# Kernel tuning notes

Measured on AMD Instinct MI355X. Metric: run time of the kernel, lower is better.

Reference implementation:

```python
import jax, jax.numpy as jnp
import numpy as np

B, H, S, D = 4, 8, 8192, 64


def setup_inputs() -> dict:
    key = jax.random.key(0)
    kq, kk, kv_, kqm, kkm = jax.random.split(key, 5)
    q = jax.random.normal(kq, (B, H, S, D), dtype=jnp.float32)
    k = jax.random.normal(kk, (B, H, S, D), dtype=jnp.float32)
    v = jax.random.normal(kv_, (B, H, S, D), dtype=jnp.float32)
    q_mask = jax.random.randint(kqm, (B, S), 0, 2).astype(jnp.bool_)
    kv_mask = jax.random.randint(kkm, (B, S), 0, 2).astype(jnp.bool_)
    return {"q": q, "k": k, "v": v, "q_mask": q_mask, "kv_mask": kv_mask}


def reference(q, k, v, q_mask, kv_mask):
    # Linear (kernelized) attention branch: feature map phi(x) = elu(x) + 1
    qe = jax.nn.elu(q) + 1.0
    ke = jax.nn.elu(k) + 1.0
    qm = q_mask.astype(q.dtype)[:, None, :, None]   # [B,1,S,1]
    km = kv_mask.astype(q.dtype)[:, None, :, None]
    qe = qe * qm
    ke = ke * km
    ve = v * km
    s = v.shape[2]
    # kv: [B,H,D,D] contraction over kv sequence
    kv = jnp.einsum('bhsd,bhsc->bhdc', ke, ve / s)
    # normalizer per query position: [B,H,L]
    div = 1.0 / (jnp.einsum('bhld,bhsd->bhl', qe, ke) + 1e-6)
    out = s * jnp.einsum('bhld,bhdc,bhl->bhlc', qe, kv, div)
    return out
```

## Files before the change

### kernel.cpp

```cpp
#include <hip/hip_runtime.h>


#define S_LEN 8192
#define NBH 32
#define KVSTRIDE 4160
#define NCHUNK 16
#define K3_XB 16

typedef __attribute__((ext_vector_type(4))) float f32x4;

__device__ __forceinline__ float elu1(float x) {
  return x > 0.0f ? (x + 1.0f) : __expf(x);
}

__global__ __launch_bounds__(256) void k1_partial(
    const float* __restrict__ kin, const float* __restrict__ vin,
    const int* __restrict__ kv_mask, float* __restrict__ partials, int seg_rows) {
  __shared__ float ke_lds[2][64 * 64];
  __shared__ float ve_lds[2][64 * 64];
  const int tid = threadIdx.x;
  const int seg = blockIdx.x, bh = blockIdx.y, b = bh >> 3;
  const int rbase = seg * seg_rows;
  const int dg = tid >> 4, cg = tid & 15;
  const float* kbase = kin + (size_t)bh * S_LEN * 64;
  const float* vbase = vin + (size_t)bh * S_LEN * 64;
  const int* mbase = kv_mask + b * S_LEN;

  f32x4 kr[4], vr[4];
  float mr[4];
  float acc[4][4];
#pragma unroll
  for (int i = 0; i < 4; ++i)
#pragma unroll
    for (int j = 0; j < 4; ++j) acc[i][j] = 0.f;
  f32x4 ksump = {0.f, 0.f, 0.f, 0.f};

#define LOAD_T(r0_)                                                    \
  {                                                                    \
    const float* kp_ = kbase + (size_t)(r0_) * 64;                     \
    const float* vp_ = vbase + (size_t)(r0_) * 64;                     \
    _Pragma("unroll")                                                  \
    for (int i_ = 0; i_ < 4; ++i_) {                                   \
      int f_ = tid + 256 * i_;                                         \
      kr[i_] = *(const f32x4*)(kp_ + (size_t)f_ * 4);                  \
      vr[i_] = *(const f32x4*)(vp_ + (size_t)f_ * 4);                  \
      mr[i_] = mbase[(r0_) + dg + 16 * i_] ? 1.0f : 0.0f;              \
    }                                                                  \
  }

#define STORE_T(buf_)                                                  \
  {                                                                    \
    _Pragma("unroll")                                                  \
    for (int i_ = 0; i_ < 4; ++i_) {                                   \
      int row_ = dg + 16 * i_;                                         \
      float m_ = mr[i_];                                               \
      float mv_ = m_ * (1.0f / 8192.0f);                               \
      f32x4 ke4_, ve4_;                                                \
      _Pragma("unroll")                                                \
      for (int j_ = 0; j_ < 4; ++j_) {                                 \
        ke4_[j_] = elu1(kr[i_][j_]) * m_;                              \
        ve4_[j_] = vr[i_][j_] * mv_;                                   \
      }                                                                \
      ksump += ke4_;                                                   \
      *(f32x4*)&ke_lds[buf_][row_ * 64 + cg * 4] = ke4_;               \
      *(f32x4*)&ve_lds[buf_][row_ * 64 + cg * 4] = ve4_;               \
    }                                                                  \
  }

#define COMPUTE_T(buf_)                                                \
  {                                                                    \
    _Pragma("unroll 4")                                                \
    for (int s_ = 0; s_ < 64; ++s_) {                                  \
      f32x4 kd_ = *(const f32x4*)&ke_lds[buf_][s_ * 64 + dg * 4];      \
      f32x4 vc_ = *(const f32x4*)&ve_lds[buf_][s_ * 64 + cg * 4];      \
      _Pragma("unroll")                                                \
      for (int i_ = 0; i_ < 4; ++i_)                                   \
        _Pragma("unroll")                                              \
        for (int j_ = 0; j_ < 4; ++j_)                                 \
          acc[i_][j_] = fmaf(kd_[i_], vc_[j_], acc[i_][j_]);           \
    }                                                                  \
  }

  const int ntiles = seg_rows >> 6;
  LOAD_T(rbase)
  STORE_T(0)
  for (int t = 0; t < ntiles; ++t) {
    __syncthreads();
    if (t + 1 < ntiles) LOAD_T(rbase + (t + 1) * 64)
    COMPUTE_T(t & 1)
    if (t + 1 < ntiles) STORE_T((t + 1) & 1)
  }

  float* p = partials + ((size_t)bh * gridDim.x + seg) * KVSTRIDE;
#pragma unroll
  for (int i = 0; i < 4; ++i) {
    f32x4 o;
#pragma unroll
    for (int j = 0; j < 4; ++j) o[j] = acc[i][j];
    *(f32x4*)&p[(dg * 4 + i) * 64 + cg * 4] = o;
  }
  __syncthreads();
  *(f32x4*)&ke_lds[0][tid * 4] = ksump;
  __syncthreads();
  if (tid < 64) {
    float s = 0.f;
#pragma unroll
    for (int g = 0; g < 16; ++g)
      s += ke_lds[0][(g * 16 + (tid >> 2)) * 4 + (tid & 3)];
    p[4096 + tid] = s;
  }
#undef LOAD_T
#undef STORE_T
#undef COMPUTE_T
}

__global__ __launch_bounds__(256) void k2_reduce(
    const float* __restrict__ partials, float* __restrict__ kvg, int nchunk) {
  const int idx = blockIdx.x * 256 + threadIdx.x;
  if (idx >= NBH * KVSTRIDE) return;
  const int bh = idx / KVSTRIDE;
  const int e = idx - bh * KVSTRIDE;
  const float* p = partials + (size_t)bh * nchunk * KVSTRIDE + e;
  float s0 = 0.f, s1 = 0.f, s2 = 0.f, s3 = 0.f;
  int c = 0;
  for (; c + 4 <= nchunk; c += 4) {
    s0 += p[(size_t)(c + 0) * KVSTRIDE];
    s1 += p[(size_t)(c + 1) * KVSTRIDE];
    s2 += p[(size_t)(c + 2) * KVSTRIDE];
    s3 += p[(size_t)(c + 3) * KVSTRIDE];
  }
  for (; c < nchunk; ++c) s0 += p[(size_t)c * KVSTRIDE];
  kvg[idx] = (s0 + s1) + (s2 + s3);
}

__global__ __launch_bounds__(256) void k3_out(
    const float* __restrict__ qin, const int* __restrict__ q_mask,
    const float* __restrict__ kvg, float* __restrict__ out) {
  __shared__ float kv_lds[64 * 64];
  __shared__ float qe_lds[2][64 * 68];
  __shared__ float ks_lds[64];
  const int tid = threadIdx.x;
  const int xb = blockIdx.x, bh = blockIdx.y, b = bh >> 3;
  const int lg = tid >> 4, cg = tid & 15;
  const float* kvb = kvg + (size_t)bh * KVSTRIDE;
  const float* qb = qin + (size_t)bh * S_LEN * 64;
  const int* mb = q_mask + b * S_LEN;

#pragma unroll
  for (int i = 0; i < 4; ++i) {
    int f = tid + 256 * i;
    *(f32x4*)&kv_lds[f * 4] = *(const f32x4*)(kvb + (size_t)f * 4);
  }
  if (tid < 64) ks_lds[tid] = kvb[4096 + tid];

  f32x4 qr[4];
  float mr[4];

#define LOADQ(r0_)                                                     \
  {                                                                    \
    const float* qp_ = qb + (size_t)(r0_) * 64;                        \
    _Pragma("unroll")                                                  \
    for (int i_ = 0; i_ < 4; ++i_) {                                   \
      int f_ = tid + 256 * i_;                                         \
      qr[i_] = *(const f32x4*)(qp_ + (size_t)f_ * 4);                  \
      mr[i_] = mb[(r0_) + lg + 16 * i_] ? 1.0f : 0.0f;                 \
    }                                                                  \
  }

#define STOREQ(buf_)                                                   \
  {                                                                    \
    _Pragma("unroll")                                                  \
    for (int i_ = 0; i_ < 4; ++i_) {                                   \
      int row_ = lg + 16 * i_;                                         \
      float m_ = mr[i_];                                               \
      f32x4 qe_;                                                       \
      _Pragma("unroll")                                                \
      for (int j_ = 0; j_ < 4; ++j_) qe_[j_] = elu1(qr[i_][j_]) * m_;  \
      *(f32x4*)&qe_lds[buf_][row_ * 68 + cg * 4] = qe_;                \
    }                                                                  \
  }

  const int c0 = xb * 8;
  LOADQ(c0 * 64)
  STOREQ(0)
  for (int t = 0; t < 8; ++t) {
    __syncthreads();
    if (t + 1 < 8) LOADQ((c0 + t + 1) * 64)
    float acc[4][4];
    float den[4];
#pragma unroll
    for (int il = 0; il < 4; ++il) {
      den[il] = 0.f;
#pragma unroll
      for (int j = 0; j < 4; ++j) acc[il][j] = 0.f;
    }
    const float* qbuf = qe_lds[t & 1];
#pragma unroll 8
    for (int d = 0; d < 64; d += 2) {
      float2 ksv = *(const float2*)&ks_lds[d];
      f32x4 kv0 = *(const f32x4*)&kv_lds[d * 64 + cg * 4];
      f32x4 kv1 = *(const f32x4*)&kv_lds[(d + 1) * 64 + cg * 4];
#pragma unroll
      for (int il = 0; il < 4; ++il) {
        float2 qv = *(const float2*)&qbuf[(lg * 4 + il) * 68 + d];
        den[il] = fmaf(qv.x, ksv.x, fmaf(qv.y, ksv.y, den[il]));
#pragma unroll
        for (int j = 0; j < 4; ++j)
          acc[il][j] = fmaf(qv.x, kv0[j], fmaf(qv.y, kv1[j], acc[il][j]));
      }
    }
    if (t + 1 < 8) STOREQ((t + 1) & 1)
    const int r0 = (c0 + t) * 64;
#pragma unroll
    for (int il = 0; il < 4; ++il) {
      float inv = 8192.0f / (den[il] + 1e-6f);
      int row = r0 + lg * 4 + il;
      f32x4 o;
#pragma unroll
      for (int j = 0; j < 4; ++j) o[j] = acc[il][j] * inv;
      *(f32x4*)(out + ((size_t)bh * S_LEN + row) * 64 + cg * 4) = o;
    }
  }
#undef LOADQ
#undef STOREQ
}

extern "C" void kernel_launch(void* const* d_in, const int* in_sizes, int n_in,
                              void* d_out, int out_size, void* d_ws, size_t ws_size,
                              hipStream_t stream) {
  const float* q = (const float*)d_in[0];
  const float* k = (const float*)d_in[1];
  const float* v = (const float*)d_in[2];
  const int* qm = (const int*)d_in[3];
  const int* km = (const int*)d_in[4];
  float* out = (float*)d_out;

  int nchunk = NCHUNK;
  while (nchunk > 1) {
    size_t need = (size_t)NBH * nchunk * KVSTRIDE * 4 + (size_t)NBH * KVSTRIDE * 4;
    if (need <= ws_size) break;
    nchunk >>= 1;
  }
  float* partials = (float*)d_ws;
  float* kvg = partials + (size_t)NBH * nchunk * KVSTRIDE;
  int seg_rows = S_LEN / nchunk;

  k1_partial<<<dim3(nchunk, NBH), 256, 0, stream>>>(k, v, km, partials, seg_rows);
  int n_elem = NBH * KVSTRIDE;
  k2_reduce<<<dim3((n_elem + 255) / 256), 256, 0, stream>>>(partials, kvg, nchunk);
  k3_out<<<dim3(K3_XB, NBH), 256, 0, stream>>>(q, qm, kvg, out);
}
```

Measured before the change: 267.4 us.

## Single-buffer LDS and double grid blocks to raise occupancy in k1/k3

Replaces the double-buffered LDS tiles in the partial-KV and output kernels with single buffers, which adds an extra barrier per tile. It doubles the number of sequence chunks and output blocks per head and sets launch bounds to 4 blocks per CU. The goal is more resident blocks and more parallelism to hide global load latency. In exchange it loses the LDS double-buffer overlap, adds synchronization, and doubles the partials that the reduce kernel must sum.

```diff
diff --git a/kernel.cpp b/kernel.cpp
--- a/kernel.cpp
+++ b/kernel.cpp
@@ -4,8 +4,8 @@
 #define S_LEN 8192
 #define NBH 32
 #define KVSTRIDE 4160
-#define NCHUNK 16
-#define K3_XB 16
+#define NCHUNK 32
+#define K3_XB 32
 
 typedef __attribute__((ext_vector_type(4))) float f32x4;
 
@@ -13,11 +13,11 @@
   return x > 0.0f ? (x + 1.0f) : __expf(x);
 }
 
-__global__ __launch_bounds__(256) void k1_partial(
+__global__ __launch_bounds__(256, 4) void k1_partial(
     const float* __restrict__ kin, const float* __restrict__ vin,
     const int* __restrict__ kv_mask, float* __restrict__ partials, int seg_rows) {
-  __shared__ float ke_lds[2][64 * 64];
-  __shared__ float ve_lds[2][64 * 64];
+  __shared__ float ke_lds[64 * 64];
+  __shared__ float ve_lds[64 * 64];
   const int tid = threadIdx.x;
   const int seg = blockIdx.x, bh = blockIdx.y, b = bh >> 3;
   const int rbase = seg * seg_rows;
@@ -48,7 +48,7 @@
     }                                                                  \
   }
 
-#define STORE_T(buf_)                                                  \
+#define STORE_T()                                                      \
   {                                                                    \
     _Pragma("unroll")                                                  \
     for (int i_ = 0; i_ < 4; ++i_) {                                   \
@@ -62,17 +62,17 @@
         ve4_[j_] = vr[i_][j_] * mv_;                                   \
       }                                                                \
       ksump += ke4_;                                                   \
-      *(f32x4*)&ke_lds[buf_][row_ * 64 + cg * 4] = ke4_;               \
-      *(f32x4*)&ve_lds[buf_][row_ * 64 + cg * 4] = ve4_;               \
-    }                                                                  \
-  }
-
-#define COMPUTE_T(buf_)                                                \
+      *(f32x4*)&ke_lds[row_ * 64 + cg * 4] = ke4_;                     \
+      *(f32x4*)&ve_lds[row_ * 64 + cg * 4] = ve4_;                     \
+    }                                                                  \
+  }
+
+#define COMPUTE_T()                                                    \
   {                                                                    \
     _Pragma("unroll 4")                                                \
     for (int s_ = 0; s_ < 64; ++s_) {                                  \
-      f32x4 kd_ = *(const f32x4*)&ke_lds[buf_][s_ * 64 + dg * 4];      \
-      f32x4 vc_ = *(const f32x4*)&ve_lds[buf_][s_ * 64 + cg * 4];      \
+      f32x4 kd_ = *(const f32x4*)&ke_lds[s_ * 64 + dg * 4];            \
+      f32x4 vc_ = *(const f32x4*)&ve_lds[s_ * 64 + cg * 4];            \
       _Pragma("unroll")                                                \
       for (int i_ = 0; i_ < 4; ++i_)                                   \
         _Pragma("unroll")                                              \
@@ -83,12 +83,12 @@
 
   const int ntiles = seg_rows >> 6;
   LOAD_T(rbase)
-  STORE_T(0)
   for (int t = 0; t < ntiles; ++t) {
+    if (t) __syncthreads();
+    STORE_T()
     __syncthreads();
     if (t + 1 < ntiles) LOAD_T(rbase + (t + 1) * 64)
-    COMPUTE_T(t & 1)
-    if (t + 1 < ntiles) STORE_T((t + 1) & 1)
+    COMPUTE_T()
   }
 
   float* p = partials + ((size_t)bh * gridDim.x + seg) * KVSTRIDE;
@@ -100,13 +100,13 @@
     *(f32x4*)&p[(dg * 4 + i) * 64 + cg * 4] = o;
   }
   __syncthreads();
-  *(f32x4*)&ke_lds[0][tid * 4] = ksump;
+  *(f32x4*)&ke_lds[tid * 4] = ksump;
   __syncthreads();
   if (tid < 64) {
     float s = 0.f;
 #pragma unroll
     for (int g = 0; g < 16; ++g)
-      s += ke_lds[0][(g * 16 + (tid >> 2)) * 4 + (tid & 3)];
+      s += ke_lds[(g * 16 + (tid >> 2)) * 4 + (tid & 3)];
     p[4096 + tid] = s;
   }
 #undef LOAD_T
@@ -133,11 +133,11 @@
   kvg[idx] = (s0 + s1) + (s2 + s3);
 }
 
-__global__ __launch_bounds__(256) void k3_out(
+__global__ __launch_bounds__(256, 4) void k3_out(
     const float* __restrict__ qin, const int* __restrict__ q_mask,
     const float* __restrict__ kvg, float* __restrict__ out) {
   __shared__ float kv_lds[64 * 64];
-  __shared__ float qe_lds[2][64 * 68];
+  __shared__ float qe_lds[64 * 68];
   __shared__ float ks_lds[64];
   const int tid = threadIdx.x;
   const int xb = blockIdx.x, bh = blockIdx.y, b = bh >> 3;
@@ -167,7 +167,7 @@
     }                                                                  \
   }
 
-#define STOREQ(buf_)                                                   \
+#define STOREQ()                                                       \
   {                                                                    \
     _Pragma("unroll")                                                  \
     for (int i_ = 0; i_ < 4; ++i_) {                                   \
@@ -176,16 +176,17 @@
       f32x4 qe_;                                                       \
       _Pragma("unroll")                                                \
       for (int j_ = 0; j_ < 4; ++j_) qe_[j_] = elu1(qr[i_][j_]) * m_;  \
-      *(f32x4*)&qe_lds[buf_][row_ * 68 + cg * 4] = qe_;                \
-    }                                                                  \
-  }
-
-  const int c0 = xb * 8;
+      *(f32x4*)&qe_lds[row_ * 68 + cg * 4] = qe_;                      \
+    }                                                                  \
+  }
+
+  const int c0 = xb * 4;
   LOADQ(c0 * 64)
-  STOREQ(0)
-  for (int t = 0; t < 8; ++t) {
+  for (int t = 0; t < 4; ++t) {
+    if (t) __syncthreads();
+    STOREQ()
     __syncthreads();
-    if (t + 1 < 8) LOADQ((c0 + t + 1) * 64)
+    if (t + 1 < 4) LOADQ((c0 + t + 1) * 64)
     float acc[4][4];
     float den[4];
 #pragma unroll
@@ -194,7 +195,6 @@
 #pragma unroll
       for (int j = 0; j < 4; ++j) acc[il][j] = 0.f;
     }
-    const float* qbuf = qe_lds[t & 1];
 #pragma unroll 8
     for (int d = 0; d < 64; d += 2) {
       float2 ksv = *(const float2*)&ks_lds[d];
@@ -202,14 +202,13 @@
       f32x4 kv1 = *(const f32x4*)&kv_lds[(d + 1) * 64 + cg * 4];
 #pragma unroll
       for (int il = 0; il < 4; ++il) {
-        float2 qv = *(const float2*)&qbuf[(lg * 4 + il) * 68 + d];
+        float2 qv = *(const float2*)&qe_lds[(lg * 4 + il) * 68 + d];
         den[il] = fmaf(qv.x, ksv.x, fmaf(qv.y, ksv.y, den[il]));
 #pragma unroll
         for (int j = 0; j < 4; ++j)
           acc[il][j] = fmaf(qv.x, kv0[j], fmaf(qv.y, kv1[j], acc[il][j]));
       }
     }
-    if (t + 1 < 8) STOREQ((t + 1) & 1)
     const int r0 = (c0 + t) * 64;
 #pragma unroll
     for (int il = 0; il < 4; ++il) {
```

Measured after the change: 255.7 us. 4.4% less time.
